# Kernel optimization log

Hardware: AMD Instinct MI355X
Metric: run time of the kernel (lower is better)

## Reference

```python
import jax, jax.numpy as jnp
import numpy as np

S, N, H, E, L = 2048, 32, 512, 256, 2


def setup_inputs() -> dict:
    key = jax.random.key(0)
    ks = jax.random.split(key, 16)
    s = 0.05  # weight scale for stability
    return {
        "x": jax.random.randint(ks[0], (N,), 0, 10),
        "encoder_states": jax.random.normal(ks[1], (S, N, 2 * H), jnp.float32),
        "hidden": jax.random.normal(ks[2], (L, N, H), jnp.float32),
        "cell": jax.random.normal(ks[3], (L, N, H), jnp.float32),
        "W_energy": jax.random.normal(ks[4], (1, 3 * H), jnp.float32) * s,
        "b_energy": jnp.zeros((1,), jnp.float32),
        "emb_table": jax.random.normal(ks[5], (10, E), jnp.float32),
        "wih0": jax.random.normal(ks[6], (4 * H, 2 * H + E), jnp.float32) * s,
        "whh0": jax.random.normal(ks[7], (4 * H, H), jnp.float32) * s,
        "bih0": jnp.zeros((4 * H,), jnp.float32),
        "bhh0": jnp.zeros((4 * H,), jnp.float32),
        "wih1": jax.random.normal(ks[8], (4 * H, H), jnp.float32) * s,
        "whh1": jax.random.normal(ks[9], (4 * H, H), jnp.float32) * s,
        "bih1": jnp.zeros((4 * H,), jnp.float32),
        "bhh1": jnp.zeros((4 * H,), jnp.float32),
        "Wc": jax.random.normal(ks[10], (10, H), jnp.float32) * s,
        "bc": jnp.zeros((10,), jnp.float32),
    }


def _lstm_cell(x, h, c, wih, whh, bih, bhh):
    # PyTorch gate order: i, f, g, o
    gates = x @ wih.T + bih + h @ whh.T + bhh  # [N, 4H]
    i, f, g, o = jnp.split(gates, 4, axis=-1)
    c_new = jax.nn.sigmoid(f) * c + jax.nn.sigmoid(i) * jnp.tanh(g)
    h_new = jax.nn.sigmoid(o) * jnp.tanh(c_new)
    return h_new, c_new


def reference(x, encoder_states, hidden, cell, W_energy, b_energy, emb_table,
              wih0, whh0, bih0, bhh0, wih1, whh1, bih1, bhh1, Wc, bc):
    seq_len = encoder_states.shape[0]
    h_last = hidden[-1]  # [N, H]
    h_rep = jnp.broadcast_to(h_last, (seq_len,) + h_last.shape)  # [S, N, H]
    cat = jnp.concatenate([h_rep, encoder_states], axis=2)  # [S, N, 3H]
    energy = jax.nn.relu(cat @ W_energy.T + b_energy)  # [S, N, 1]
    attn = jax.nn.softmax(energy, axis=0)  # softmax over seq dim
    context = jnp.einsum('snk,snl->knl', attn, encoder_states)  # [1, N, 2H]
    emb = emb_table[x][None]  # [1, N, E]
    inp = jnp.concatenate([context, emb], axis=2)[0]  # [N, 2H+E]
    h0, c0 = _lstm_cell(inp, hidden[0], cell[0], wih0, whh0, bih0, bhh0)
    h1, c1 = _lstm_cell(h0, hidden[1], cell[1], wih1, whh1, bih1, bhh1)
    predictions = h1 @ Wc.T + bc  # [N, 10]
    hidden_new = jnp.stack([h0, h1], axis=0)
    cell_new = jnp.stack([c0, c1], axis=0)
    return predictions, hidden_new, cell_new
```

## Files before the change

### kernel.cpp

```cpp
#include <hip/hip_runtime.h>

#define SS 2048
#define NN_ 32
#define HH 512
#define EE 256
#define TWO_H 1024

#define OUT_PRED 0
#define OUT_H0 320
#define OUT_H1 16704
#define OUT_C0 33088
#define OUT_C1 49472

#define WS_ACC 0
#define WS_SUMW 2097152
#define WS_XCAT0 2099200
#define WS_PG0 0
#define WS_XCAT1 2156544
#define WS_PG1 2189312

__device__ __forceinline__ float wave_reduce(float v) {
  v += __shfl_xor(v, 32);
  v += __shfl_xor(v, 16);
  v += __shfl_xor(v, 8);
  v += __shfl_xor(v, 4);
  v += __shfl_xor(v, 2);
  v += __shfl_xor(v, 1);
  return v;
}

__device__ __forceinline__ float sigmoidf_(float x) { return 1.0f / (1.0f + __expf(-x)); }

__global__ __launch_bounds__(256, 8) void attn_pass(
    const float* __restrict__ enc, const float* __restrict__ hidden,
    const float* __restrict__ We, const float* __restrict__ be,
    float* __restrict__ ws) {
  const int blk = blockIdx.x;
  const int n = blk >> 6;
  const int chunk = blk & 63;
  const int t = threadIdx.x;
  const int wave = t >> 6;
  const int lane = t & 63;

  const float* hl = hidden + (size_t)(NN_ + n) * HH;
  float cp;
  {
    float4 a = *(const float4*)(hl + lane * 8);
    float4 b = *(const float4*)(hl + lane * 8 + 4);
    float4 wa = *(const float4*)(We + lane * 8);
    float4 wb = *(const float4*)(We + lane * 8 + 4);
    cp = a.x * wa.x + a.y * wa.y + a.z * wa.z + a.w * wa.w +
         b.x * wb.x + b.y * wb.y + b.z * wb.z + b.w * wb.w;
  }
  cp = wave_reduce(cp);
  const float c_n = cp + be[0];

  const float4 w0 = *(const float4*)(We + HH + 0 * 256 + lane * 4);
  const float4 w1 = *(const float4*)(We + HH + 1 * 256 + lane * 4);
  const float4 w2 = *(const float4*)(We + HH + 2 * 256 + lane * 4);
  const float4 w3 = *(const float4*)(We + HH + 3 * 256 + lane * 4);

  float4 acc0 = {0, 0, 0, 0}, acc1 = {0, 0, 0, 0}, acc2 = {0, 0, 0, 0}, acc3 = {0, 0, 0, 0};
  float sumw = 0.f;

  const int sBase = chunk * 32 + wave * 8;
#pragma unroll 2
  for (int i = 0; i < 8; ++i) {
    const float* row = enc + ((size_t)(sBase + i) * NN_ + n) * TWO_H;
    float4 e0 = *(const float4*)(row + 0 * 256 + lane * 4);
    float4 e1 = *(const float4*)(row + 1 * 256 + lane * 4);
    float4 e2 = *(const float4*)(row + 2 * 256 + lane * 4);
    float4 e3 = *(const float4*)(row + 3 * 256 + lane * 4);
    float d = e0.x * w0.x + e0.y * w0.y + e0.z * w0.z + e0.w * w0.w +
              e1.x * w1.x + e1.y * w1.y + e1.z * w1.z + e1.w * w1.w +
              e2.x * w2.x + e2.y * w2.y + e2.z * w2.z + e2.w * w2.w +
              e3.x * w3.x + e3.y * w3.y + e3.z * w3.z + e3.w * w3.w;
    d = wave_reduce(d);
    float en = c_n + d;
    en = en > 0.f ? en : 0.f;
    float p = __expf(en - 4.0f);
    sumw += p;
    acc0.x = fmaf(p, e0.x, acc0.x); acc0.y = fmaf(p, e0.y, acc0.y);
    acc0.z = fmaf(p, e0.z, acc0.z); acc0.w = fmaf(p, e0.w, acc0.w);
    acc1.x = fmaf(p, e1.x, acc1.x); acc1.y = fmaf(p, e1.y, acc1.y);
    acc1.z = fmaf(p, e1.z, acc1.z); acc1.w = fmaf(p, e1.w, acc1.w);
    acc2.x = fmaf(p, e2.x, acc2.x); acc2.y = fmaf(p, e2.y, acc2.y);
    acc2.z = fmaf(p, e2.z, acc2.z); acc2.w = fmaf(p, e2.w, acc2.w);
    acc3.x = fmaf(p, e3.x, acc3.x); acc3.y = fmaf(p, e3.y, acc3.y);
    acc3.z = fmaf(p, e3.z, acc3.z); acc3.w = fmaf(p, e3.w, acc3.w);
  }

  __shared__ __align__(16) float lacc[4][1024];
  __shared__ float lsum[4];
  *(float4*)&lacc[wave][0 * 256 + lane * 4] = acc0;
  *(float4*)&lacc[wave][1 * 256 + lane * 4] = acc1;
  *(float4*)&lacc[wave][2 * 256 + lane * 4] = acc2;
  *(float4*)&lacc[wave][3 * 256 + lane * 4] = acc3;
  if (lane == 0) lsum[wave] = sumw;
  __syncthreads();

  const int j = t * 4;
  float4 o;
  o.x = lacc[0][j + 0] + lacc[1][j + 0] + lacc[2][j + 0] + lacc[3][j + 0];
  o.y = lacc[0][j + 1] + lacc[1][j + 1] + lacc[2][j + 1] + lacc[3][j + 1];
  o.z = lacc[0][j + 2] + lacc[1][j + 2] + lacc[2][j + 2] + lacc[3][j + 2];
  o.w = lacc[0][j + 3] + lacc[1][j + 3] + lacc[2][j + 3] + lacc[3][j + 3];
  *(float4*)&ws[WS_ACC + (size_t)blk * 1024 + j] = o;
  if (t == 0) ws[WS_SUMW + blk] = lsum[0] + lsum[1] + lsum[2] + lsum[3];
}

__global__ __launch_bounds__(256) void reduce_ctx(
    const int* __restrict__ x, const float* __restrict__ emb,
    const float* __restrict__ hidden, float* __restrict__ ws) {
  const int b = blockIdx.x;
  const int n = b >> 3;
  const int jg = b & 7;
  const int t = threadIdx.x;
  if (t < 128) {
    const int j = jg * 128 + t;
    float sumw = 0.f;
#pragma unroll
    for (int c = 0; c < 64; ++c) sumw += ws[WS_SUMW + n * 64 + c];
    const float inv = 1.0f / sumw;
    float v = 0.f;
#pragma unroll 8
    for (int c = 0; c < 64; ++c) v += ws[WS_ACC + (size_t)(n * 64 + c) * 1024 + j];
    ws[WS_XCAT0 + j * NN_ + n] = v * inv;
  } else if (t < 224) {
    const int row = jg * 96 + (t - 128);
    float v;
    if (row < 256) {
      v = emb[(size_t)x[n] * EE + row];
    } else {
      v = hidden[(size_t)n * HH + (row - 256)];
    }
    ws[WS_XCAT0 + (1024 + row) * NN_ + n] = v;
  }
}

__global__ __launch_bounds__(256, 2) void gates0_kernel(
    const float* __restrict__ wih0, const float* __restrict__ whh0, float* __restrict__ ws) {
  __shared__ __align__(16) float xs[256 * 32];
  __shared__ __align__(16) float wt[32 * 260];
  const int bid = blockIdx.x;
  const int chunk = bid % 7;
  const int hg = bid / 7;
  const int t = threadIdx.x;
  const int nn = t & 31;
  const int rl = t >> 5;

  {
    const float* src = ws + WS_XCAT0 + (size_t)chunk * 256 * 32;
#pragma unroll
    for (int i = t * 4; i < 8192; i += 1024)
      *(float4*)&xs[i] = *(const float4*)&src[i];
  }
  {
    const int r = t >> 3;
    const int k8 = t & 7;
    const int grow = (r >> 3) * 512 + hg * 8 + (r & 7);
    const float* src = (chunk < 5) ? (wih0 + (size_t)grow * 1280 + chunk * 256)
                                   : (whh0 + (size_t)grow * 512 + (chunk - 5) * 256);
#pragma unroll
    for (int jj = 0; jj < 8; ++jj) {
      const int kl = jj * 32 + k8 * 4;
      *(float4*)&wt[r * 260 + kl] = *(const float4*)(src + kl);
    }
  }
  __syncthreads();

  const float* w0p = &wt[(0 * 8 + rl) * 260];
  const float* w1p = &wt[(1 * 8 + rl) * 260];
  const float* w2p = &wt[(2 * 8 + rl) * 260];
  const float* w3p = &wt[(3 * 8 + rl) * 260];

  float a0 = 0.f, a1 = 0.f, a2 = 0.f, a3 = 0.f;
#pragma unroll 4
  for (int k = 0; k < 256; k += 4) {
    const float4 w0 = *(const float4*)(w0p + k);
    const float4 w1 = *(const float4*)(w1p + k);
    const float4 w2 = *(const float4*)(w2p + k);
    const float4 w3 = *(const float4*)(w3p + k);
    const float x0 = xs[(k + 0) * 32 + nn];
    const float x1 = xs[(k + 1) * 32 + nn];
    const float x2 = xs[(k + 2) * 32 + nn];
    const float x3 = xs[(k + 3) * 32 + nn];
    a0 += w0.x * x0 + w0.y * x1 + w0.z * x2 + w0.w * x3;
    a1 += w1.x * x0 + w1.y * x1 + w1.z * x2 + w1.w * x3;
    a2 += w2.x * x0 + w2.y * x1 + w2.z * x2 + w2.w * x3;
    a3 += w3.x * x0 + w3.y * x1 + w3.z * x2 + w3.w * x3;
  }

  const int h = hg * 8 + rl;
  float* dst = ws + WS_PG0 + ((size_t)chunk * 2048 + h) * 32 + nn;
  dst[0 * 512 * 32] = a0;
  dst[1 * 512 * 32] = a1;
  dst[2 * 512 * 32] = a2;
  dst[3 * 512 * 32] = a3;
}

__global__ __launch_bounds__(256) void lstm0_kernel(
    const float* __restrict__ cell, const float* __restrict__ hidden,
    const float* __restrict__ bih0, const float* __restrict__ bhh0,
    float* __restrict__ out, float* __restrict__ ws) {
  const int g = blockIdx.x * 256 + threadIdx.x;
  const int nn = g & 31;
  const int h = g >> 5;
  float gi = bih0[h] + bhh0[h];
  float gf = bih0[512 + h] + bhh0[512 + h];
  float gg = bih0[1024 + h] + bhh0[1024 + h];
  float go = bih0[1536 + h] + bhh0[1536 + h];
#pragma unroll
  for (int c = 0; c < 7; ++c) {
    const float* p = ws + WS_PG0 + (size_t)c * 2048 * 32;
    gi += p[(0 * 512 + h) * 32 + nn];
    gf += p[(1 * 512 + h) * 32 + nn];
    gg += p[(2 * 512 + h) * 32 + nn];
    go += p[(3 * 512 + h) * 32 + nn];
  }
  const float cprev = cell[(size_t)nn * HH + h];
  const float c0 = sigmoidf_(gf) * cprev + sigmoidf_(gi) * tanhf(gg);
  const float h0 = sigmoidf_(go) * tanhf(c0);
  out[OUT_H0 + nn * HH + h] = h0;
  out[OUT_C0 + nn * HH + h] = c0;
  ws[WS_XCAT1 + h * 32 + nn] = h0;
  ws[WS_XCAT1 + (512 + h) * 32 + nn] = hidden[(size_t)(NN_ + nn) * HH + h];
}

__global__ __launch_bounds__(256, 2) void gates1_kernel(
    const float* __restrict__ wih1, const float* __restrict__ whh1, float* __restrict__ ws) {
  __shared__ __align__(16) float xs[128 * 32];
  __shared__ __align__(16) float wt[32 * 132];
  const int bid = blockIdx.x;
  const int chunk = bid & 7;
  const int hg = bid >> 3;
  const int t = threadIdx.x;
  const int nn = t & 31;
  const int rl = t >> 5;
  const int kb = chunk * 128;

  {
    const float* src = ws + WS_XCAT1 + (size_t)kb * 32;
#pragma unroll
    for (int i = t * 4; i < 4096; i += 1024)
      *(float4*)&xs[i] = *(const float4*)&src[i];
  }
  {
    const int r = t >> 3;
    const int k8 = t & 7;
    const int grow = (r >> 3) * 512 + hg * 8 + (r & 7);
    const float* src = (chunk < 4) ? (wih1 + (size_t)grow * 512 + kb)
                                   : (whh1 + (size_t)grow * 512 + (kb - 512));
#pragma unroll
    for (int jj = 0; jj < 4; ++jj) {
      const int kl = jj * 32 + k8 * 4;
      *(float4*)&wt[r * 132 + kl] = *(const float4*)(src + kl);
    }
  }
  __syncthreads();

  const float* w0p = &wt[(0 * 8 + rl) * 132];
  const float* w1p = &wt[(1 * 8 + rl) * 132];
  const float* w2p = &wt[(2 * 8 + rl) * 132];
  const float* w3p = &wt[(3 * 8 + rl) * 132];

  float a0 = 0.f, a1 = 0.f, a2 = 0.f, a3 = 0.f;
#pragma unroll 4
  for (int k = 0; k < 128; k += 4) {
    const float4 w0 = *(const float4*)(w0p + k);
    const float4 w1 = *(const float4*)(w1p + k);
    const float4 w2 = *(const float4*)(w2p + k);
    const float4 w3 = *(const float4*)(w3p + k);
    const float x0 = xs[(k + 0) * 32 + nn];
    const float x1 = xs[(k + 1) * 32 + nn];
    const float x2 = xs[(k + 2) * 32 + nn];
    const float x3 = xs[(k + 3) * 32 + nn];
    a0 += w0.x * x0 + w0.y * x1 + w0.z * x2 + w0.w * x3;
    a1 += w1.x * x0 + w1.y * x1 + w1.z * x2 + w1.w * x3;
    a2 += w2.x * x0 + w2.y * x1 + w2.z * x2 + w2.w * x3;
    a3 += w3.x * x0 + w3.y * x1 + w3.z * x2 + w3.w * x3;
  }

  const int h = hg * 8 + rl;
  float* dst = ws + WS_PG1 + ((size_t)chunk * 2048 + h) * 32 + nn;
  dst[0 * 512 * 32] = a0;
  dst[1 * 512 * 32] = a1;
  dst[2 * 512 * 32] = a2;
  dst[3 * 512 * 32] = a3;
}

__global__ __launch_bounds__(256) void lstm1_kernel(
    const float* __restrict__ cell,
    const float* __restrict__ bih1, const float* __restrict__ bhh1,
    float* __restrict__ out, float* __restrict__ ws) {
  const int g = blockIdx.x * 256 + threadIdx.x;
  const int nn = g & 31;
  const int h = g >> 5;
  float gi = bih1[h] + bhh1[h];
  float gf = bih1[512 + h] + bhh1[512 + h];
  float gg = bih1[1024 + h] + bhh1[1024 + h];
  float go = bih1[1536 + h] + bhh1[1536 + h];
#pragma unroll
  for (int c = 0; c < 8; ++c) {
    const float* p = ws + WS_PG1 + (size_t)c * 2048 * 32;
    gi += p[(0 * 512 + h) * 32 + nn];
    gf += p[(1 * 512 + h) * 32 + nn];
    gg += p[(2 * 512 + h) * 32 + nn];
    go += p[(3 * 512 + h) * 32 + nn];
  }
  const float cprev = cell[(size_t)(NN_ + nn) * HH + h];
  const float c1 = sigmoidf_(gf) * cprev + sigmoidf_(gi) * tanhf(gg);
  const float h1 = sigmoidf_(go) * tanhf(c1);
  out[OUT_H1 + nn * HH + h] = h1;
  out[OUT_C1 + nn * HH + h] = c1;
}

__global__ __launch_bounds__(256) void pred_kernel(
    const float* __restrict__ Wc, const float* __restrict__ bc, float* out) {
  const int wid = blockIdx.x * 4 + (threadIdx.x >> 6);
  const int lane = threadIdx.x & 63;
  const int nn = wid / 10;
  const int c = wid % 10;
  const float* hp = out + OUT_H1 + (size_t)nn * HH;
  const float* wp = Wc + (size_t)c * HH;
  float p = 0.f;
#pragma unroll
  for (int j = 0; j < 8; ++j) p += hp[lane * 8 + j] * wp[lane * 8 + j];
  p = wave_reduce(p);
  if (lane == 0) out[OUT_PRED + nn * 10 + c] = p + bc[c];
}

extern "C" void kernel_launch(void* const* d_in, const int* in_sizes, int n_in,
                              void* d_out, int out_size, void* d_ws, size_t ws_size,
                              hipStream_t stream) {
  const int* x = (const int*)d_in[0];
  const float* enc = (const float*)d_in[1];
  const float* hidden = (const float*)d_in[2];
  const float* cell = (const float*)d_in[3];
  const float* We = (const float*)d_in[4];
  const float* be = (const float*)d_in[5];
  const float* emb = (const float*)d_in[6];
  const float* wih0 = (const float*)d_in[7];
  const float* whh0 = (const float*)d_in[8];
  const float* bih0 = (const float*)d_in[9];
  const float* bhh0 = (const float*)d_in[10];
  const float* wih1 = (const float*)d_in[11];
  const float* whh1 = (const float*)d_in[12];
  const float* bih1 = (const float*)d_in[13];
  const float* bhh1 = (const float*)d_in[14];
  const float* Wc = (const float*)d_in[15];
  const float* bc = (const float*)d_in[16];
  float* out = (float*)d_out;
  float* ws = (float*)d_ws;

  hipLaunchKernelGGL(attn_pass, dim3(2048), dim3(256), 0, stream, enc, hidden, We, be, ws);
  hipLaunchKernelGGL(reduce_ctx, dim3(256), dim3(256), 0, stream, x, emb, hidden, ws);
  hipLaunchKernelGGL(gates0_kernel, dim3(448), dim3(256), 0, stream, wih0, whh0, ws);
  hipLaunchKernelGGL(lstm0_kernel, dim3(64), dim3(256), 0, stream, cell, hidden, bih0, bhh0, out, ws);
  hipLaunchKernelGGL(gates1_kernel, dim3(512), dim3(256), 0, stream, wih1, whh1, ws);
  hipLaunchKernelGGL(lstm1_kernel, dim3(64), dim3(256), 0, stream, cell, bih1, bhh1, out, ws);
  hipLaunchKernelGGL(pred_kernel, dim3(80), dim3(256), 0, stream, Wc, bc, out);
}
```

Measured before the change: 80.18 us.

## Give each wave its own batch index in attention pass, drop LDS reduction

The attention pass now launches 256 blocks of 512 threads, and each wave handles one batch index over 32 sequence rows. Previously four waves split those rows for a single batch index and combined their partials through shared memory. Each wave now writes its partial accumulator and weight sum directly to the workspace, which removes the LDS round trip and the barrier. The trade-off is fewer blocks and longer serial loops per wave, which may hurt latency hiding on an 8-block-per-CU budget now capped at 2 blocks per CU.

```diff
diff --git a/kernel.cpp b/kernel.cpp
--- a/kernel.cpp
+++ b/kernel.cpp
@@ -31,16 +31,17 @@
 
 __device__ __forceinline__ float sigmoidf_(float x) { return 1.0f / (1.0f + __expf(-x)); }
 
-__global__ __launch_bounds__(256, 8) void attn_pass(
+__global__ __launch_bounds__(512, 2) void attn_pass(
     const float* __restrict__ enc, const float* __restrict__ hidden,
     const float* __restrict__ We, const float* __restrict__ be,
     float* __restrict__ ws) {
   const int blk = blockIdx.x;
-  const int n = blk >> 6;
+  const int ng = blk >> 6;
   const int chunk = blk & 63;
   const int t = threadIdx.x;
   const int wave = t >> 6;
   const int lane = t & 63;
+  const int n = ng * 8 + wave;
 
   const float* hl = hidden + (size_t)(NN_ + n) * HH;
   float cp;
@@ -63,14 +64,16 @@
   float4 acc0 = {0, 0, 0, 0}, acc1 = {0, 0, 0, 0}, acc2 = {0, 0, 0, 0}, acc3 = {0, 0, 0, 0};
   float sumw = 0.f;
 
-  const int sBase = chunk * 32 + wave * 8;
+  const int sBase = chunk * 32;
+  const float* base = enc + ((size_t)sBase * NN_ + n) * TWO_H + lane * 4;
+
 #pragma unroll 2
-  for (int i = 0; i < 8; ++i) {
-    const float* row = enc + ((size_t)(sBase + i) * NN_ + n) * TWO_H;
-    float4 e0 = *(const float4*)(row + 0 * 256 + lane * 4);
-    float4 e1 = *(const float4*)(row + 1 * 256 + lane * 4);
-    float4 e2 = *(const float4*)(row + 2 * 256 + lane * 4);
-    float4 e3 = *(const float4*)(row + 3 * 256 + lane * 4);
+  for (int i = 0; i < 32; ++i) {
+    const float* row = base + (size_t)i * (NN_ * TWO_H);
+    float4 e0 = *(const float4*)(row + 0 * 256);
+    float4 e1 = *(const float4*)(row + 1 * 256);
+    float4 e2 = *(const float4*)(row + 2 * 256);
+    float4 e3 = *(const float4*)(row + 3 * 256);
     float d = e0.x * w0.x + e0.y * w0.y + e0.z * w0.z + e0.w * w0.w +
               e1.x * w1.x + e1.y * w1.y + e1.z * w1.z + e1.w * w1.w +
               e2.x * w2.x + e2.y * w2.y + e2.z * w2.z + e2.w * w2.w +
@@ -90,23 +93,13 @@
     acc3.z = fmaf(p, e3.z, acc3.z); acc3.w = fmaf(p, e3.w, acc3.w);
   }
 
-  __shared__ __align__(16) float lacc[4][1024];
-  __shared__ float lsum[4];
-  *(float4*)&lacc[wave][0 * 256 + lane * 4] = acc0;
-  *(float4*)&lacc[wave][1 * 256 + lane * 4] = acc1;
-  *(float4*)&lacc[wave][2 * 256 + lane * 4] = acc2;
-  *(float4*)&lacc[wave][3 * 256 + lane * 4] = acc3;
-  if (lane == 0) lsum[wave] = sumw;
-  __syncthreads();
-
-  const int j = t * 4;
-  float4 o;
-  o.x = lacc[0][j + 0] + lacc[1][j + 0] + lacc[2][j + 0] + lacc[3][j + 0];
-  o.y = lacc[0][j + 1] + lacc[1][j + 1] + lacc[2][j + 1] + lacc[3][j + 1];
-  o.z = lacc[0][j + 2] + lacc[1][j + 2] + lacc[2][j + 2] + lacc[3][j + 2];
-  o.w = lacc[0][j + 3] + lacc[1][j + 3] + lacc[2][j + 3] + lacc[3][j + 3];
-  *(float4*)&ws[WS_ACC + (size_t)blk * 1024 + j] = o;
-  if (t == 0) ws[WS_SUMW + blk] = lsum[0] + lsum[1] + lsum[2] + lsum[3];
+  const int pidx = n * 64 + chunk;
+  float* dst = ws + WS_ACC + (size_t)pidx * 1024 + lane * 4;
+  *(float4*)(dst + 0 * 256) = acc0;
+  *(float4*)(dst + 1 * 256) = acc1;
+  *(float4*)(dst + 2 * 256) = acc2;
+  *(float4*)(dst + 3 * 256) = acc3;
+  if (lane == 0) ws[WS_SUMW + pidx] = sumw;
 }
 
 __global__ __launch_bounds__(256) void reduce_ctx(
@@ -353,7 +346,7 @@
   float* out = (float*)d_out;
   float* ws = (float*)d_ws;
 
-  hipLaunchKernelGGL(attn_pass, dim3(2048), dim3(256), 0, stream, enc, hidden, We, be, ws);
+  hipLaunchKernelGGL(attn_pass, dim3(256), dim3(512), 0, stream, enc, hidden, We, be, ws);
   hipLaunchKernelGGL(reduce_ctx, dim3(256), dim3(256), 0, stream, x, emb, hidden, ws);
   hipLaunchKernelGGL(gates0_kernel, dim3(448), dim3(256), 0, stream, wih0, whh0, ws);
   hipLaunchKernelGGL(lstm0_kernel, dim3(64), dim3(256), 0, stream, cell, hidden, bih0, bhh0, out, ws);
```

New measurement: 79.65 us. Within noise of the previous version (-0.7%).
